# Kernel tuning notes

Measured on AMD Instinct MI355X. Metric: run time of the kernel, lower is better.

The kernel has to match this reference:

```python
import jax, jax.numpy as jnp
import numpy as np

NUM_LEVELS = 2
RADIUS = 3


def setup_inputs() -> dict:
    key = jax.random.key(0)
    k1, k2, k3 = jax.random.split(key, 3)
    x = jax.random.normal(k1, (4, 320, 9, 32, 32), dtype=jnp.float32)
    w_fc0 = jax.random.normal(k2, (160, 320), dtype=jnp.float32) * 0.05
    w_fc1 = jax.random.normal(k3, (160, 320), dtype=jnp.float32) * 0.05
    return {"x": x, "w_fc0": w_fc0, "w_fc1": w_fc1}


def _bilinear_zeros(img, xs, ys):
    # img: (M, H, W); xs, ys: (M, K) pixel coords.
    # Matches F.grid_sample(mode='bilinear', padding_mode='zeros', align_corners=True):
    # align_corners normalization round-trips to the raw pixel coords, and
    # out-of-bounds corners contribute zero.
    M, H, W = img.shape
    x0f = jnp.floor(xs)
    y0f = jnp.floor(ys)
    wx = xs - x0f
    wy = ys - y0f
    x0 = x0f.astype(jnp.int32)
    y0 = y0f.astype(jnp.int32)
    x1 = x0 + 1
    y1 = y0 + 1
    n = jnp.arange(M)[:, None]

    def corner(yi, xi):
        valid = (xi >= 0) & (xi < W) & (yi >= 0) & (yi < H)
        v = img[n, jnp.clip(yi, 0, H - 1), jnp.clip(xi, 0, W - 1)]
        return v * valid.astype(img.dtype)

    v00 = corner(y0, x0)
    v01 = corner(y0, x1)
    v10 = corner(y1, x0)
    v11 = corner(y1, x1)
    return (v00 * (1 - wx) * (1 - wy) + v01 * wx * (1 - wy)
            + v10 * (1 - wx) * wy + v11 * wx * wy)


def reference(x, w_fc0, w_fc1):
    b, c, T, h, w = x.shape
    xt = jnp.transpose(x, (0, 2, 1, 3, 4))  # (b, T, c, h, w)
    # 1x1 convs (no bias) on consecutive-frame pairs
    f0 = jnp.einsum('btchw,oc->bothw', xt[:, :-1], w_fc0)
    f1 = jnp.einsum('btchw,oc->bothw', xt[:, 1:], w_fc1)
    t = T - 1
    c2 = w_fc0.shape[0]
    f0 = f0.reshape(b * t, c2, h * w)
    f1 = f1.reshape(b * t, c2, h * w)
    # all-pairs correlation volume, normalized by channel count
    corr = jnp.einsum('nci,ncj->nij', f0, f1) / c2  # (bt, hw, hw)
    corr = corr.reshape(b * t * h * w, h, w)

    # pyramid via 2x2 avg pooling
    pyramid = [corr]
    for _ in range(NUM_LEVELS - 1):
        M, H, W = pyramid[-1].shape
        pyramid.append(pyramid[-1].reshape(M, H // 2, 2, W // 2, 2).mean(axis=(2, 4)))

    # per-pixel centroids (x, y), tiled over the bt batch axis
    ys, xs = jnp.meshgrid(jnp.arange(h), jnp.arange(w), indexing='ij')
    cx = jnp.tile(xs.reshape(-1).astype(jnp.float32), b * t)  # (bt*h*w,)
    cy = jnp.tile(ys.reshape(-1).astype(jnp.float32), b * t)

    # delta[i, j] = (d[i], d[j]); delta[...,0] -> x offset, delta[...,1] -> y offset
    r = RADIUS
    d = jnp.linspace(-r, r, 2 * r + 1)
    dx = jnp.repeat(d, 2 * r + 1)  # varies along first window dim
    dy = jnp.tile(d, 2 * r + 1)    # varies along second window dim

    outs = []
    for i, ci in enumerate(pyramid):
        xs_s = cx[:, None] / (2 ** i) + dx[None, :]  # (M, K)
        ys_s = cy[:, None] / (2 ** i) + dy[None, :]
        v = _bilinear_zeros(ci, xs_s, ys_s)          # (M, (2r+1)^2)
        outs.append(v.reshape(b * t, h, w, -1))
    out = jnp.concatenate(outs, axis=3)              # (bt, h, w, L*(2r+1)^2)
    out = out.reshape(b, t, h, w, -1)
    return jnp.transpose(out, (0, 4, 1, 2, 3)).astype(jnp.float32)
```

## Files before the change

kernel.cpp:

```cpp
#include <hip/hip_runtime.h>
#include <hip/hip_bf16.h>

typedef __attribute__((ext_vector_type(8))) short short8;
typedef __attribute__((ext_vector_type(4))) float f32x4;

static constexpr int HW = 1024;
static constexpr int C2 = 160;
static constexpr int FS = 168;
static constexpr int WPLANE = 160 * 40;
static constexpr int WKS = 4 * WPLANE;
static constexpr int KSTEPS = 10;
static constexpr size_t PL = 32ull * 1024 * 160;
static constexpr size_t PPL = 32ull * 256 * 160;

__device__ inline short bfh(float v) {
  __hip_bfloat16 h = __float2bfloat16(v);
  return *reinterpret_cast<short*>(&h);
}
__device__ inline float bff(short s) {
  union { unsigned u; float f; } c;
  c.u = ((unsigned)(unsigned short)s) << 16;
  return c.f;
}
__device__ inline unsigned packhl(float v0, float v1, unsigned& lo) {
  const short h0 = bfh(v0), h1 = bfh(v1);
  const short l0 = bfh(v0 - bff(h0)), l1 = bfh(v1 - bff(h1));
  lo = (unsigned)(unsigned short)l0 | ((unsigned)(unsigned short)l1 << 16);
  return (unsigned)(unsigned short)h0 | ((unsigned)(unsigned short)h1 << 16);
}

__global__ __launch_bounds__(256)
void wprep_kernel(const float* __restrict__ w0, const float* __restrict__ w1,
                  short* __restrict__ wp) {
  const int id = blockIdx.x * 256 + threadIdx.x;
  if (id >= KSTEPS * WKS) return;
  const int kk = id % 40;
  const int o = (id / 40) % 160;
  const int hl = (id / 6400) % 2;
  const int mat = (id / 12800) % 2;
  const int ks = id / 25600;
  short outv = 0;
  if (kk < 32) {
    const float v = (mat ? w1 : w0)[o * 320 + ks * 32 + kk];
    const short hb = bfh(v);
    outv = hl ? bfh(v - bff(hb)) : hb;
  }
  wp[id] = outv;
}

__global__ __launch_bounds__(256)
void conv_fused(const float* __restrict__ x, const short* __restrict__ wprep,
                short* __restrict__ f0bh, short* __restrict__ f0bl,
                short* __restrict__ f1bh, short* __restrict__ f1bl) {
  __shared__ __align__(16) short xB[2][288 * 40];
  __shared__ __align__(16) short aL[2][80 * 40];
  const int pxt = blockIdx.x;
  const int qp = blockIdx.y;
  const int bb = blockIdx.z;
  const int tid = threadIdx.x;
  const int lane = tid & 63;
  const int wave = __builtin_amdgcn_readfirstlane(tid >> 6);
  const int lr = lane & 15, kg = lane >> 4;
  const int pxh = wave & 1;
  const int fpar = wave >> 1;

  f32x4 acc[5][5];
#pragma unroll
  for (int mt = 0; mt < 5; ++mt)
#pragma unroll
    for (int fi = 0; fi < 5; ++fi)
#pragma unroll
      for (int r = 0; r < 4; ++r) acc[mt][fi][r] = 0.f;

  const size_t xbase = (size_t)bb * 320 * 9216 + (size_t)pxt * 32;

  for (int ks = 0; ks < KSTEPS; ++ks) {
    __syncthreads();
#pragma unroll
    for (int i = 0; i < 4; ++i) {
      const int idx = tid + i * 256;
      if (idx < 800) {
        const int u = idx % 5, gr = (idx / 5) % 80, hl = idx / 400;
        const int mat = gr >= 40;
        const int o = qp * 40 + (gr - mat * 40);
        const uint4* s = reinterpret_cast<const uint4*>(
            wprep + (size_t)((ks * 2 + mat) * 2 + hl) * WPLANE + o * 40) + u;
        reinterpret_cast<uint4*>(&aL[hl][gr * 40])[u] = *s;
      }
    }
#pragma unroll
    for (int i = 0; i < 18; ++i) {
      const int id = tid + i * 256;
      const int px = id & 31, f = (id >> 5) % 9, kl2 = id / 288;
      const float* xp =
          x + xbase + (size_t)(ks * 32 + 2 * kl2) * 9216 + f * 1024 + px;
      const float v0 = xp[0], v1 = xp[9216];
      unsigned lo;
      const unsigned hp = packhl(v0, v1, lo);
      *reinterpret_cast<unsigned*>(&xB[0][(f * 32 + px) * 40 + 2 * kl2]) = hp;
      *reinterpret_cast<unsigned*>(&xB[1][(f * 32 + px) * 40 + 2 * kl2]) = lo;
    }
    __syncthreads();
    short8 Ah[5], Al[5];
#pragma unroll
    for (int mt = 0; mt < 5; ++mt) {
      Ah[mt] = *reinterpret_cast<const short8*>(&aL[0][(mt * 16 + lr) * 40 + kg * 8]);
      Al[mt] = *reinterpret_cast<const short8*>(&aL[1][(mt * 16 + lr) * 40 + kg * 8]);
    }
#pragma unroll
    for (int fi = 0; fi < 5; ++fi) {
      if (2 * fi + fpar < 9) {
        const int f = 2 * fi + fpar;
        const int col = (f * 32 + pxh * 16 + lr) * 40 + kg * 8;
        const short8 Bh = *reinterpret_cast<const short8*>(&xB[0][col]);
        const short8 Bl = *reinterpret_cast<const short8*>(&xB[1][col]);
#pragma unroll
        for (int mt = 0; mt < 5; ++mt) {
          acc[mt][fi] = __builtin_amdgcn_mfma_f32_16x16x32_bf16(Ah[mt], Bh, acc[mt][fi], 0, 0, 0);
          acc[mt][fi] = __builtin_amdgcn_mfma_f32_16x16x32_bf16(Ah[mt], Bl, acc[mt][fi], 0, 0, 0);
          acc[mt][fi] = __builtin_amdgcn_mfma_f32_16x16x32_bf16(Al[mt], Bh, acc[mt][fi], 0, 0, 0);
        }
      }
    }
  }

  short* tL = &xB[0][0];
#pragma unroll
  for (int m = 0; m < 2; ++m) {
    __syncthreads();
#pragma unroll
    for (int mt = 0; mt < 5; ++mt)
#pragma unroll
      for (int fi = 0; fi < 5; ++fi) {
        const int f = 2 * fi + fpar;
        const int tt = f - m;
        if (f < 9 && (unsigned)tt < 8u) {
#pragma unroll
          for (int rr = 0; rr < 4; ++rr) {
            const int gr = mt * 16 + kg * 4 + rr;
            if ((gr >= 40) == (m == 1)) {
              const int rowl = gr - m * 40;
              const int ql = rowl / 20, r20 = rowl % 20;
              const int c = 8 * r20 + tt;
              const int row = ql * 32 + pxh * 16 + lr;
              const float v = acc[mt][fi][rr];
              const short h = bfh(v);
              const short l = bfh(v - bff(h));
              tL[row * FS + c] = h;
              tL[10752 + row * FS + c] = l;
            }
          }
        }
      }
    __syncthreads();
#pragma unroll
    for (int i = 0; i < 10; ++i) {
      const int idx = tid + i * 256;
      const int plane = idx / 1280, rem = idx % 1280;
      const int row = rem / 20, c16 = rem % 20;
      const int ql = row >> 5, pxl = row & 31;
      const int n = bb * 8 + qp * 2 + ql;
      short* dst = (m == 0) ? (plane ? f0bl : f0bh) : (plane ? f1bl : f1bh);
      *reinterpret_cast<uint4*>(dst + ((size_t)n * 1024 + pxt * 32 + pxl) * 160 + c16 * 8) =
          *reinterpret_cast<const uint4*>(&tL[plane * 10752 + row * FS + c16 * 8]);
    }
  }
}

__global__ __launch_bounds__(256)
void pool_b(const short* __restrict__ f1bh, const short* __restrict__ f1bl,
            short* __restrict__ g1pbh, short* __restrict__ g1pbl) {
  const int id = blockIdx.x * 256 + threadIdx.x;
  if (id >= 32 * 256 * 20) return;
  const int c16 = id % 20;
  const int PX = (id / 20) & 255;
  const int n = id / (20 * 256);
  const int Y = PX >> 4, X = PX & 15;
  const int r0 = Y * 64 + X * 2;
  const size_t base = ((size_t)n * 1024 + r0) * 160 + c16 * 8;
  const short8 h00 = *reinterpret_cast<const short8*>(f1bh + base);
  const short8 h01 = *reinterpret_cast<const short8*>(f1bh + base + 160);
  const short8 h10 = *reinterpret_cast<const short8*>(f1bh + base + 32 * 160);
  const short8 h11 = *reinterpret_cast<const short8*>(f1bh + base + 33 * 160);
  const short8 l00 = *reinterpret_cast<const short8*>(f1bl + base);
  const short8 l01 = *reinterpret_cast<const short8*>(f1bl + base + 160);
  const short8 l10 = *reinterpret_cast<const short8*>(f1bl + base + 32 * 160);
  const short8 l11 = *reinterpret_cast<const short8*>(f1bl + base + 33 * 160);
  short8 ho, lo;
#pragma unroll
  for (int j = 0; j < 8; ++j) {
    const float v = 0.25f * ((bff(h00[j]) + bff(l00[j])) + (bff(h01[j]) + bff(l01[j])) +
                             (bff(h10[j]) + bff(l10[j])) + (bff(h11[j]) + bff(l11[j])));
    const short h = bfh(v);
    ho[j] = h;
    lo[j] = bfh(v - bff(h));
  }
  const size_t ob = ((size_t)n * 256 + PX) * 160 + c16 * 8;
  *reinterpret_cast<short8*>(g1pbh + ob) = ho;
  *reinterpret_cast<short8*>(g1pbl + ob) = lo;
}

__global__ __launch_bounds__(256)
void corr_kernel(const short* __restrict__ f0bh, const short* __restrict__ f0bl,
                 const short* __restrict__ f1bh, const short* __restrict__ f1bl,
                 const short* __restrict__ g1pbh, const short* __restrict__ g1pbl,
                 float* __restrict__ out) {
  __shared__ __align__(16) short f0L[2][32 * FS];
  __shared__ __align__(16) short f1L[2][32 * FS];
  __shared__ float S0[32 * 33];
  __shared__ float S1[2][32 * 17];
  const int flat = blockIdx.x;
  const int xcd = flat & 7;
  const int rr_ = flat >> 3;
  const int y = rr_ & 31;
  const int n = (xcd << 2) | (rr_ >> 5);
  const int bb = n >> 3, q = n & 7;
  const int tid = threadIdx.x;
  const int lane = tid & 63;
  const int wave = __builtin_amdgcn_readfirstlane(tid >> 6);
  const int lr = lane & 15, kg = lane >> 4;
  const int xx = tid & 31;
  const int hi = tid >> 5;
  const float inv = 1.f / 160.f;
  const size_t obase = (size_t)(bb * 784 + q) * 1024 + (size_t)y * 32;

#pragma unroll
  for (int i = 0; i < 5; ++i) {
    const int idx = tid + i * 256;
    const int plane = idx / 640, rem = idx % 640;
    const int px = rem / 20, c16 = rem % 20;
    const short* src = (plane ? f0bl : f0bh) + ((size_t)n * 1024 + y * 32 + px) * 160 + c16 * 8;
    *reinterpret_cast<uint4*>(&f0L[plane][px * FS + c16 * 8]) =
        *reinterpret_cast<const uint4*>(src);
  }
  __syncthreads();

  const int mi0 = wave >> 1, ni0 = wave & 1;
  short8 a0h[5], a0l[5];
#pragma unroll
  for (int ks = 0; ks < 5; ++ks) {
    a0h[ks] = *reinterpret_cast<const short8*>(&f0L[0][(mi0 * 16 + lr) * FS + ks * 32 + kg * 8]);
    a0l[ks] = *reinterpret_cast<const short8*>(&f0L[1][(mi0 * 16 + lr) * FS + ks * 32 + kg * 8]);
  }

  for (int dyi = 0; dyi < 7; ++dyi) {
    const int yy = y + dyi - 3;
    const bool inr = (unsigned)yy < 32u;
    __syncthreads();
    if (inr) {
#pragma unroll
      for (int i = 0; i < 5; ++i) {
        const int idx = tid + i * 256;
        const int plane = idx / 640, rem = idx % 640;
        const int px = rem / 20, c16 = rem % 20;
        const short* src = (plane ? f1bl : f1bh) + ((size_t)n * 1024 + yy * 32 + px) * 160 + c16 * 8;
        *reinterpret_cast<uint4*>(&f1L[plane][px * FS + c16 * 8]) =
            *reinterpret_cast<const uint4*>(src);
      }
    }
    __syncthreads();
    if (inr) {
      f32x4 aA = {0.f, 0.f, 0.f, 0.f}, aB = aA, aC = aA;
#pragma unroll
      for (int ks = 0; ks < 5; ++ks) {
        const short8 bh = *reinterpret_cast<const short8*>(&f1L[0][(ni0 * 16 + lr) * FS + ks * 32 + kg * 8]);
        const short8 bl = *reinterpret_cast<const short8*>(&f1L[1][(ni0 * 16 + lr) * FS + ks * 32 + kg * 8]);
        aA = __builtin_amdgcn_mfma_f32_16x16x32_bf16(a0h[ks], bh, aA, 0, 0, 0);
        aB = __builtin_amdgcn_mfma_f32_16x16x32_bf16(a0h[ks], bl, aB, 0, 0, 0);
        aC = __builtin_amdgcn_mfma_f32_16x16x32_bf16(a0l[ks], bh, aC, 0, 0, 0);
      }
#pragma unroll
      for (int r = 0; r < 4; ++r)
        S0[(mi0 * 16 + kg * 4 + r) * 33 + ni0 * 16 + lr] = (aA[r] + aB[r]) + aC[r];
    }
    __syncthreads();
    if (hi < 7) {
      const int x2 = xx + hi - 3;
      const float val = (inr && (unsigned)x2 < 32u) ? S0[xx * 33 + x2] * inv : 0.f;
      out[obase + (size_t)(hi * 7 + dyi) * 8192 + xx] = val;
    }
  }

  short8 a1h[5], a1l[5];
  if (wave < 2) {
#pragma unroll
    for (int ks = 0; ks < 5; ++ks) {
      a1h[ks] = *reinterpret_cast<const short8*>(&f0L[0][(wave * 16 + lr) * FS + ks * 32 + kg * 8]);
      a1l[ks] = *reinterpret_cast<const short8*>(&f0L[1][(wave * 16 + lr) * FS + ks * 32 + kg * 8]);
    }
  }
  const int Y0 = (y >> 1) - 3;
  const float wy = (y & 1) ? 0.5f : 0.f;
  for (int v = 0; v < 8; ++v) {
    const int Y = Y0 + v;
    const bool inr = (unsigned)Y < 16u;
    __syncthreads();
    if (inr) {
#pragma unroll
      for (int i = 0; i < 3; ++i) {
        const int idx = tid + i * 256;
        if (idx < 640) {
          const int plane = idx / 320, rem = idx % 320;
          const int px = rem / 20, c16 = rem % 20;
          const short* src = (plane ? g1pbl : g1pbh) + ((size_t)n * 256 + Y * 16 + px) * 160 + c16 * 8;
          *reinterpret_cast<uint4*>(&f1L[plane][px * FS + c16 * 8]) =
              *reinterpret_cast<const uint4*>(src);
        }
      }
    }
    __syncthreads();
    if (wave < 2) {
      f32x4 aA = {0.f, 0.f, 0.f, 0.f}, aB = aA, aC = aA;
      if (inr) {
#pragma unroll
        for (int ks = 0; ks < 5; ++ks) {
          const short8 bh = *reinterpret_cast<const short8*>(&f1L[0][lr * FS + ks * 32 + kg * 8]);
          const short8 bl = *reinterpret_cast<const short8*>(&f1L[1][lr * FS + ks * 32 + kg * 8]);
          aA = __builtin_amdgcn_mfma_f32_16x16x32_bf16(a1h[ks], bh, aA, 0, 0, 0);
          aB = __builtin_amdgcn_mfma_f32_16x16x32_bf16(a1h[ks], bl, aB, 0, 0, 0);
          aC = __builtin_amdgcn_mfma_f32_16x16x32_bf16(a1l[ks], bh, aC, 0, 0, 0);
        }
      }
#pragma unroll
      for (int r = 0; r < 4; ++r)
        S1[v & 1][(wave * 16 + kg * 4 + r) * 17 + lr] = (aA[r] + aB[r]) + aC[r];
    }
    __syncthreads();
    if (v >= 1 && hi < 7) {
      const int dyi = v - 1;
      const int Xl = (xx >> 1) - 3 + hi;
      const int Xr = Xl + 1;
      const float* t0 = S1[(v - 1) & 1];
      const float* t1 = S1[v & 1];
      const float a00 = ((unsigned)Xl < 16u) ? t0[xx * 17 + Xl] : 0.f;
      const float a01 = ((unsigned)Xr < 16u) ? t0[xx * 17 + Xr] : 0.f;
      const float a10 = ((unsigned)Xl < 16u) ? t1[xx * 17 + Xl] : 0.f;
      const float a11 = ((unsigned)Xr < 16u) ? t1[xx * 17 + Xr] : 0.f;
      const float wx = (xx & 1) ? 0.5f : 0.f;
      const float val = ((1.f - wx) * ((1.f - wy) * a00 + wy * a10) +
                         wx * ((1.f - wy) * a01 + wy * a11)) * inv;
      out[obase + (size_t)(49 + hi * 7 + dyi) * 8192 + xx] = val;
    }
  }
}

extern "C" void kernel_launch(void* const* d_in, const int* in_sizes, int n_in,
                              void* d_out, int out_size, void* d_ws,
                              size_t ws_size, hipStream_t stream) {
  const float* x = (const float*)d_in[0];
  const float* w0 = (const float*)d_in[1];
  const float* w1 = (const float*)d_in[2];
  short* f0bh = (short*)d_ws;
  short* f0bl = f0bh + PL;
  short* f1bh = f0bl + PL;
  short* f1bl = f1bh + PL;
  short* g1pbh = f1bl + PL;
  short* g1pbl = g1pbh + PPL;
  short* wprep = g1pbh;
  float* out = (float*)d_out;

  wprep_kernel<<<1000, 256, 0, stream>>>(w0, w1, wprep);
  conv_fused<<<dim3(32, 4, 4), 256, 0, stream>>>(x, wprep, f0bh, f0bl, f1bh, f1bl);
  pool_b<<<640, 256, 0, stream>>>(f1bh, f1bl, g1pbh, g1pbl);
  corr_kernel<<<1024, 256, 0, stream>>>(f0bh, f0bl, f1bh, f1bl, g1pbh, g1pbl, out);
}
```

Baseline: 94.94 us.

## Restructure conv into smaller output-channel tiles with fp32 LDS staging and split-on-read

The conv kernel now gives each block 20 output channels per matrix instead of 40, doubling the grid to 32x8x4 blocks. The input is staged in LDS as raw fp32 with float4 loads and an XOR swizzle, and the bf16 hi/lo split happens when B fragments are read, not when they are stored. Weight fragments are read directly from global memory instead of through LDS. This aims to raise occupancy and cut LDS traffic and staging work, at the cost of re-reading x once per extra block and wasting part of the third M tile (48 rows for 40 outputs).

Measured after the change: 138.2 us. +45.6%, slower.

```diff
diff --git a/kernel.cpp b/kernel.cpp
--- a/kernel.cpp
+++ b/kernel.cpp
@@ -21,12 +21,6 @@
   union { unsigned u; float f; } c;
   c.u = ((unsigned)(unsigned short)s) << 16;
   return c.f;
-}
-__device__ inline unsigned packhl(float v0, float v1, unsigned& lo) {
-  const short h0 = bfh(v0), h1 = bfh(v1);
-  const short l0 = bfh(v0 - bff(h0)), l1 = bfh(v1 - bff(h1));
-  lo = (unsigned)(unsigned short)l0 | ((unsigned)(unsigned short)l1 << 16);
-  return (unsigned)(unsigned short)h0 | ((unsigned)(unsigned short)h1 << 16);
 }
 
 __global__ __launch_bounds__(256)
@@ -49,13 +43,12 @@
 }
 
 __global__ __launch_bounds__(256)
-void conv_fused(const float* __restrict__ x, const short* __restrict__ wprep,
-                short* __restrict__ f0bh, short* __restrict__ f0bl,
-                short* __restrict__ f1bh, short* __restrict__ f1bl) {
-  __shared__ __align__(16) short xB[2][288 * 40];
-  __shared__ __align__(16) short aL[2][80 * 40];
+void conv_q(const float* __restrict__ x, const short* __restrict__ wprep,
+            short* __restrict__ f0bh, short* __restrict__ f0bl,
+            short* __restrict__ f1bh, short* __restrict__ f1bl) {
+  __shared__ __align__(16) float xB[9216];
   const int pxt = blockIdx.x;
-  const int qp = blockIdx.y;
+  const int q = blockIdx.y;
   const int bb = blockIdx.z;
   const int tid = threadIdx.x;
   const int lane = tid & 63;
@@ -63,73 +56,99 @@
   const int lr = lane & 15, kg = lane >> 4;
   const int pxh = wave & 1;
   const int fpar = wave >> 1;
-
-  f32x4 acc[5][5];
-#pragma unroll
-  for (int mt = 0; mt < 5; ++mt)
+  const int n = bb * 8 + q;
+
+  int aoff[3];
+#pragma unroll
+  for (int mt = 0; mt < 3; ++mt) {
+    const int gr = mt * 16 + lr;
+    const int mat = gr >= 20;
+    int r = gr - mat * 20;
+    if (r > 19) r = 19;
+    aoff[mt] = mat * 2 * WPLANE + (q * 20 + r) * 40 + kg * 8;
+  }
+  const int pxq = ((pxh * 4 + (lr >> 2)) ^ (kg << 1)) & 7;
+  const int bbase = kg * 256 + pxq * 4 + (lr & 3);
+
+  const int l8 = lane >> 3, l7 = lane & 7;
+  const float* xg = x + (size_t)bb * 320 * 9216 + (size_t)pxt * 32;
+
+  f32x4 acc[3][5];
+#pragma unroll
+  for (int mt = 0; mt < 3; ++mt)
 #pragma unroll
     for (int fi = 0; fi < 5; ++fi)
 #pragma unroll
       for (int r = 0; r < 4; ++r) acc[mt][fi][r] = 0.f;
 
-  const size_t xbase = (size_t)bb * 320 * 9216 + (size_t)pxt * 32;
-
   for (int ks = 0; ks < KSTEPS; ++ks) {
     __syncthreads();
 #pragma unroll
-    for (int i = 0; i < 4; ++i) {
-      const int idx = tid + i * 256;
-      if (idx < 800) {
-        const int u = idx % 5, gr = (idx / 5) % 80, hl = idx / 400;
-        const int mat = gr >= 40;
-        const int o = qp * 40 + (gr - mat * 40);
-        const uint4* s = reinterpret_cast<const uint4*>(
-            wprep + (size_t)((ks * 2 + mat) * 2 + hl) * WPLANE + o * 40) + u;
-        reinterpret_cast<uint4*>(&aL[hl][gr * 40])[u] = *s;
-      }
-    }
-#pragma unroll
-    for (int i = 0; i < 18; ++i) {
-      const int id = tid + i * 256;
-      const int px = id & 31, f = (id >> 5) % 9, kl2 = id / 288;
-      const float* xp =
-          x + xbase + (size_t)(ks * 32 + 2 * kl2) * 9216 + f * 1024 + px;
-      const float v0 = xp[0], v1 = xp[9216];
-      unsigned lo;
-      const unsigned hp = packhl(v0, v1, lo);
-      *reinterpret_cast<unsigned*>(&xB[0][(f * 32 + px) * 40 + 2 * kl2]) = hp;
-      *reinterpret_cast<unsigned*>(&xB[1][(f * 32 + px) * 40 + 2 * kl2]) = lo;
-    }
-    __syncthreads();
-    short8 Ah[5], Al[5];
-#pragma unroll
-    for (int mt = 0; mt < 5; ++mt) {
-      Ah[mt] = *reinterpret_cast<const short8*>(&aL[0][(mt * 16 + lr) * 40 + kg * 8]);
-      Al[mt] = *reinterpret_cast<const short8*>(&aL[1][(mt * 16 + lr) * 40 + kg * 8]);
+    for (int g = 0; g < 2; ++g) {
+      float4 xr[5];
+      const int jn = g ? 4 : 5;
+#pragma unroll
+      for (int j = 0; j < 5; ++j) {
+        if (j < jn) {
+          const int gi = wave * 9 + g * 5 + j;
+          const int f = gi >> 2, k4 = gi & 3;
+          const int kk = k4 * 8 + l8;
+          xr[j] = *reinterpret_cast<const float4*>(
+              xg + (size_t)(ks * 32 + kk) * 9216 + f * 1024 +
+              ((l7 ^ (k4 << 1)) << 2));
+        }
+      }
+#pragma unroll
+      for (int j = 0; j < 5; ++j) {
+        if (j < jn) {
+          const int gi = wave * 9 + g * 5 + j;
+          *reinterpret_cast<float4*>(xB + gi * 256 + lane * 4) = xr[j];
+        }
+      }
+    }
+    __syncthreads();
+
+    short8 Ah[3], Al[3];
+    const short* wks = wprep + (size_t)ks * WKS;
+#pragma unroll
+    for (int mt = 0; mt < 3; ++mt) {
+      Ah[mt] = *reinterpret_cast<const short8*>(wks + aoff[mt]);
+      Al[mt] = *reinterpret_cast<const short8*>(wks + aoff[mt] + WPLANE);
     }
 #pragma unroll
     for (int fi = 0; fi < 5; ++fi) {
-      if (2 * fi + fpar < 9) {
-        const int f = 2 * fi + fpar;
-        const int col = (f * 32 + pxh * 16 + lr) * 40 + kg * 8;
-        const short8 Bh = *reinterpret_cast<const short8*>(&xB[0][col]);
-        const short8 Bl = *reinterpret_cast<const short8*>(&xB[1][col]);
-#pragma unroll
-        for (int mt = 0; mt < 5; ++mt) {
-          acc[mt][fi] = __builtin_amdgcn_mfma_f32_16x16x32_bf16(Ah[mt], Bh, acc[mt][fi], 0, 0, 0);
-          acc[mt][fi] = __builtin_amdgcn_mfma_f32_16x16x32_bf16(Ah[mt], Bl, acc[mt][fi], 0, 0, 0);
-          acc[mt][fi] = __builtin_amdgcn_mfma_f32_16x16x32_bf16(Al[mt], Bh, acc[mt][fi], 0, 0, 0);
-        }
-      }
-    }
-  }
-
-  short* tL = &xB[0][0];
+      const int f = 2 * fi + fpar;
+      if (f < 9) {
+        const float* xf = xB + f * 1024 + bbase;
+        float xv[8];
+#pragma unroll
+        for (int j2 = 0; j2 < 8; ++j2) xv[j2] = xf[j2 * 32];
+        short8 Bh, Bl;
+#pragma unroll
+        for (int j2 = 0; j2 < 8; ++j2) {
+          const short h = bfh(xv[j2]);
+          Bh[j2] = h;
+          Bl[j2] = bfh(xv[j2] - bff(h));
+        }
+#pragma unroll
+        for (int mt = 0; mt < 3; ++mt) {
+          acc[mt][fi] = __builtin_amdgcn_mfma_f32_16x16x32_bf16(
+              Ah[mt], Bh, acc[mt][fi], 0, 0, 0);
+          acc[mt][fi] = __builtin_amdgcn_mfma_f32_16x16x32_bf16(
+              Ah[mt], Bl, acc[mt][fi], 0, 0, 0);
+          acc[mt][fi] = __builtin_amdgcn_mfma_f32_16x16x32_bf16(
+              Al[mt], Bh, acc[mt][fi], 0, 0, 0);
+        }
+      }
+    }
+  }
+
+  short* tL = reinterpret_cast<short*>(xB);
 #pragma unroll
   for (int m = 0; m < 2; ++m) {
     __syncthreads();
 #pragma unroll
-    for (int mt = 0; mt < 5; ++mt)
+    for (int mt = 0; mt < 3; ++mt)
 #pragma unroll
       for (int fi = 0; fi < 5; ++fi) {
         const int f = 2 * fi + fpar;
@@ -138,31 +157,29 @@
 #pragma unroll
           for (int rr = 0; rr < 4; ++rr) {
             const int gr = mt * 16 + kg * 4 + rr;
-            if ((gr >= 40) == (m == 1)) {
-              const int rowl = gr - m * 40;
-              const int ql = rowl / 20, r20 = rowl % 20;
+            const bool ok = m ? (gr >= 20 && gr < 40) : (gr < 20);
+            if (ok) {
+              const int r20 = gr - m * 20;
               const int c = 8 * r20 + tt;
-              const int row = ql * 32 + pxh * 16 + lr;
+              const int row = pxh * 16 + lr;
               const float v = acc[mt][fi][rr];
               const short h = bfh(v);
-              const short l = bfh(v - bff(h));
               tL[row * FS + c] = h;
-              tL[10752 + row * FS + c] = l;
+              tL[5376 + row * FS + c] = bfh(v - bff(h));
             }
           }
         }
       }
     __syncthreads();
 #pragma unroll
-    for (int i = 0; i < 10; ++i) {
+    for (int i = 0; i < 5; ++i) {
       const int idx = tid + i * 256;
-      const int plane = idx / 1280, rem = idx % 1280;
+      const int plane = idx / 640, rem = idx % 640;
       const int row = rem / 20, c16 = rem % 20;
-      const int ql = row >> 5, pxl = row & 31;
-      const int n = bb * 8 + qp * 2 + ql;
-      short* dst = (m == 0) ? (plane ? f0bl : f0bh) : (plane ? f1bl : f1bh);
-      *reinterpret_cast<uint4*>(dst + ((size_t)n * 1024 + pxt * 32 + pxl) * 160 + c16 * 8) =
-          *reinterpret_cast<const uint4*>(&tL[plane * 10752 + row * FS + c16 * 8]);
+      short* dst = m ? (plane ? f1bl : f1bh) : (plane ? f0bl : f0bh);
+      *reinterpret_cast<uint4*>(
+          dst + ((size_t)n * 1024 + pxt * 32 + row) * 160 + c16 * 8) =
+          *reinterpret_cast<const uint4*>(&tL[plane * 5376 + row * FS + c16 * 8]);
     }
   }
 }
@@ -360,7 +377,7 @@
   float* out = (float*)d_out;
 
   wprep_kernel<<<1000, 256, 0, stream>>>(w0, w1, wprep);
-  conv_fused<<<dim3(32, 4, 4), 256, 0, stream>>>(x, wprep, f0bh, f0bl, f1bh, f1bl);
+  conv_q<<<dim3(32, 8, 4), 256, 0, stream>>>(x, wprep, f0bh, f0bl, f1bh, f1bl);
   pool_b<<<640, 256, 0, stream>>>(f1bh, f1bl, g1pbh, g1pbl);
   corr_kernel<<<1024, 256, 0, stream>>>(f0bh, f0bl, f1bh, f1bl, g1pbh, g1pbl, out);
 }
```

## Stage conv inputs into LDS with direct global_load_lds and split bf16 at read

Applied to the files above, without the earlier changes.

The conv kernel no longer loads x through registers, splits it to bf16 hi/lo and writes to LDS. Instead it copies raw fp32 x tiles straight into LDS with global_load_lds and an XOR-swizzled layout, and does the hi/lo split while reading B fragments. Weights are pre-laid out per (ks, qp) image so they can also be copied by direct LDS loads. This cuts register staging and VALU work in the load phase, but repeats the bf16 conversion per wave at fragment-read time and uses more LDS per block.

New measurement: 82.97 us. 1.14x faster.

```diff
diff --git a/kernel.cpp b/kernel.cpp
--- a/kernel.cpp
+++ b/kernel.cpp
@@ -7,11 +7,10 @@
 static constexpr int HW = 1024;
 static constexpr int C2 = 160;
 static constexpr int FS = 168;
-static constexpr int WPLANE = 160 * 40;
-static constexpr int WKS = 4 * WPLANE;
 static constexpr int KSTEPS = 10;
 static constexpr size_t PL = 32ull * 1024 * 160;
 static constexpr size_t PPL = 32ull * 256 * 160;
+static constexpr int AIMG = 6656;
 
 __device__ inline short bfh(float v) {
   __hip_bfloat16 h = __float2bfloat16(v);
@@ -22,38 +21,45 @@
   c.u = ((unsigned)(unsigned short)s) << 16;
   return c.f;
 }
-__device__ inline unsigned packhl(float v0, float v1, unsigned& lo) {
-  const short h0 = bfh(v0), h1 = bfh(v1);
-  const short l0 = bfh(v0 - bff(h0)), l1 = bfh(v1 - bff(h1));
-  lo = (unsigned)(unsigned short)l0 | ((unsigned)(unsigned short)l1 << 16);
-  return (unsigned)(unsigned short)h0 | ((unsigned)(unsigned short)h1 << 16);
+
+typedef const __attribute__((address_space(1))) void* gas_t;
+typedef __attribute__((address_space(3))) void* las_t;
+__device__ inline void gload_lds16(const void* g, void* l) {
+  __builtin_amdgcn_global_load_lds((gas_t)g, (las_t)l, 16, 0, 0);
 }
 
 __global__ __launch_bounds__(256)
-void wprep_kernel(const float* __restrict__ w0, const float* __restrict__ w1,
-                  short* __restrict__ wp) {
+void wprep2_kernel(const float* __restrict__ w0, const float* __restrict__ w1,
+                   short* __restrict__ wp) {
   const int id = blockIdx.x * 256 + threadIdx.x;
-  if (id >= KSTEPS * WKS) return;
-  const int kk = id % 40;
-  const int o = (id / 40) % 160;
-  const int hl = (id / 6400) % 2;
-  const int mat = (id / 12800) % 2;
-  const int ks = id / 25600;
+  if (id >= KSTEPS * 4 * AIMG) return;
+  const int img = id / AIMG, r = id % AIMG;
+  const int ks = img >> 2, qp = img & 3;
   short outv = 0;
-  if (kk < 32) {
-    const float v = (mat ? w1 : w0)[o * 320 + ks * 32 + kk];
-    const short hb = bfh(v);
-    outv = hl ? bfh(v - bff(hb)) : hb;
+  if (r < 6400) {
+    const int hl = r / 3200;
+    const int g2 = r % 3200;
+    const int gr = g2 / 40, kk = g2 % 40;
+    const int mat = gr >= 40;
+    const int o = qp * 40 + gr - mat * 40;
+    if (kk < 32) {
+      const float v = (mat ? w1 : w0)[o * 320 + ks * 32 + kk];
+      const short hb = bfh(v);
+      outv = hl ? bfh(v - bff(hb)) : hb;
+    }
   }
   wp[id] = outv;
 }
 
 __global__ __launch_bounds__(256)
-void conv_fused(const float* __restrict__ x, const short* __restrict__ wprep,
+void conv_fused(const float* __restrict__ x, const short* __restrict__ wprep2,
                 short* __restrict__ f0bh, short* __restrict__ f0bl,
                 short* __restrict__ f1bh, short* __restrict__ f1bl) {
-  __shared__ __align__(16) short xB[2][288 * 40];
-  __shared__ __align__(16) short aL[2][80 * 40];
+  __shared__ __align__(16) char lds[50176];
+  float* xF = reinterpret_cast<float*>(lds);
+  short* aL = reinterpret_cast<short*>(lds + 36864);
+  short* tL = reinterpret_cast<short*>(lds);
+
   const int pxt = blockIdx.x;
   const int qp = blockIdx.y;
   const int bb = blockIdx.z;
@@ -64,6 +70,11 @@
   const int pxh = wave & 1;
   const int fpar = wave >> 1;
 
+  const int l8 = lane >> 3;
+  const int l7 = lane & 7;
+  const int px = pxh * 16 + lr;
+  const int pxs = px ^ (kg << 3);
+
   f32x4 acc[5][5];
 #pragma unroll
   for (int mt = 0; mt < 5; ++mt)
@@ -72,48 +83,50 @@
 #pragma unroll
       for (int r = 0; r < 4; ++r) acc[mt][fi][r] = 0.f;
 
-  const size_t xbase = (size_t)bb * 320 * 9216 + (size_t)pxt * 32;
+  const float* xg = x + ((size_t)(bb * 320) * 9) * 1024 + (size_t)pxt * 32;
 
   for (int ks = 0; ks < KSTEPS; ++ks) {
-    __syncthreads();
-#pragma unroll
-    for (int i = 0; i < 4; ++i) {
-      const int idx = tid + i * 256;
-      if (idx < 800) {
-        const int u = idx % 5, gr = (idx / 5) % 80, hl = idx / 400;
-        const int mat = gr >= 40;
-        const int o = qp * 40 + (gr - mat * 40);
-        const uint4* s = reinterpret_cast<const uint4*>(
-            wprep + (size_t)((ks * 2 + mat) * 2 + hl) * WPLANE + o * 40) + u;
-        reinterpret_cast<uint4*>(&aL[hl][gr * 40])[u] = *s;
-      }
-    }
-#pragma unroll
-    for (int i = 0; i < 18; ++i) {
-      const int id = tid + i * 256;
-      const int px = id & 31, f = (id >> 5) % 9, kl2 = id / 288;
-      const float* xp =
-          x + xbase + (size_t)(ks * 32 + 2 * kl2) * 9216 + f * 1024 + px;
-      const float v0 = xp[0], v1 = xp[9216];
-      unsigned lo;
-      const unsigned hp = packhl(v0, v1, lo);
-      *reinterpret_cast<unsigned*>(&xB[0][(f * 32 + px) * 40 + 2 * kl2]) = hp;
-      *reinterpret_cast<unsigned*>(&xB[1][(f * 32 + px) * 40 + 2 * kl2]) = lo;
-    }
-    __syncthreads();
+    if (ks) __syncthreads();
+    {
+      const short* src = wprep2 + (size_t)(ks * 4 + qp) * AIMG;
+#pragma unroll
+      for (int jj = 0; jj < 4; ++jj) {
+        const int j = wave * 4 + jj;
+        if (j < 13) gload_lds16(src + j * 512 + lane * 8, aL + j * 512);
+      }
+    }
+#pragma unroll
+    for (int jj = 0; jj < 9; ++jj) {
+      const int gi = wave * 9 + jj;
+      const int f = gi >> 2, oct = gi & 3;
+      const int c = ks * 32 + oct * 8 + l8;
+      const float* src =
+          xg + ((size_t)c * 9 + f) * 1024 + ((l7 ^ (oct << 1)) << 2);
+      gload_lds16(src, xF + gi * 256);
+    }
+    __syncthreads();
+
     short8 Ah[5], Al[5];
 #pragma unroll
     for (int mt = 0; mt < 5; ++mt) {
-      Ah[mt] = *reinterpret_cast<const short8*>(&aL[0][(mt * 16 + lr) * 40 + kg * 8]);
-      Al[mt] = *reinterpret_cast<const short8*>(&aL[1][(mt * 16 + lr) * 40 + kg * 8]);
+      Ah[mt] = *reinterpret_cast<const short8*>(&aL[(mt * 16 + lr) * 40 + kg * 8]);
+      Al[mt] = *reinterpret_cast<const short8*>(&aL[3200 + (mt * 16 + lr) * 40 + kg * 8]);
     }
 #pragma unroll
     for (int fi = 0; fi < 5; ++fi) {
-      if (2 * fi + fpar < 9) {
-        const int f = 2 * fi + fpar;
-        const int col = (f * 32 + pxh * 16 + lr) * 40 + kg * 8;
-        const short8 Bh = *reinterpret_cast<const short8*>(&xB[0][col]);
-        const short8 Bl = *reinterpret_cast<const short8*>(&xB[1][col]);
+      const int f = 2 * fi + fpar;
+      if (f < 9) {
+        const float* bp = xF + f * 1024 + kg * 256 + pxs;
+        float xv[8];
+#pragma unroll
+        for (int j = 0; j < 8; ++j) xv[j] = bp[j * 32];
+        short8 Bh, Bl;
+#pragma unroll
+        for (int j = 0; j < 8; ++j) {
+          const short h = bfh(xv[j]);
+          Bh[j] = h;
+          Bl[j] = bfh(xv[j] - bff(h));
+        }
 #pragma unroll
         for (int mt = 0; mt < 5; ++mt) {
           acc[mt][fi] = __builtin_amdgcn_mfma_f32_16x16x32_bf16(Ah[mt], Bh, acc[mt][fi], 0, 0, 0);
@@ -124,7 +137,6 @@
     }
   }
 
-  short* tL = &xB[0][0];
 #pragma unroll
   for (int m = 0; m < 2; ++m) {
     __syncthreads();
@@ -356,11 +368,11 @@
   short* f1bl = f1bh + PL;
   short* g1pbh = f1bl + PL;
   short* g1pbl = g1pbh + PPL;
-  short* wprep = g1pbh;
+  short* wprep2 = g1pbh;
   float* out = (float*)d_out;
 
-  wprep_kernel<<<1000, 256, 0, stream>>>(w0, w1, wprep);
-  conv_fused<<<dim3(32, 4, 4), 256, 0, stream>>>(x, wprep, f0bh, f0bl, f1bh, f1bl);
+  wprep2_kernel<<<1040, 256, 0, stream>>>(w0, w1, wprep2);
+  conv_fused<<<dim3(32, 4, 4), 256, 0, stream>>>(x, wprep2, f0bh, f0bl, f1bh, f1bl);
   pool_b<<<640, 256, 0, stream>>>(f1bh, f1bl, g1pbh, g1pbl);
   corr_kernel<<<1024, 256, 0, stream>>>(f0bh, f0bl, f1bh, f1bl, g1pbh, g1pbl, out);
 }
```
